# Performance work log

Hardware: AMD Instinct MI355X
Metric: run time of the kernel (lower is better)

The kernel has to match this reference:

```python
import jax, jax.numpy as jnp
import numpy as np

B, T, DIM, E, H = 128, 512, 256, 512, 512

def _linear_params(key, out_dim, in_dim, bias=True):
    k1, k2 = jax.random.split(key)
    bound = 1.0 / np.sqrt(in_dim)
    W = jax.random.uniform(k1, (out_dim, in_dim), jnp.float32, -bound, bound)
    if bias:
        b = jax.random.uniform(k2, (out_dim,), jnp.float32, -bound, bound)
        return W, b
    return W

def setup_inputs() -> dict:
    key = jax.random.key(0)
    ks = jax.random.split(key, 12)
    x_t = jax.random.normal(ks[0], (B, T, DIM), jnp.float32)
    h0 = jax.random.normal(ks[1], (B, H), jnp.float32)
    c0 = jax.random.normal(ks[2], (B, H), jnp.float32)
    We, be = _linear_params(ks[3], E, DIM)
    Wf, bf = _linear_params(ks[4], H, E)   # forget input proj
    Wi, bi = _linear_params(ks[5], H, E)   # input gate
    Wg, bg = _linear_params(ks[6], H, E)   # cell candidate
    Wo, bo = _linear_params(ks[7], H, E)   # output gate
    Rf = _linear_params(ks[8], H, H, bias=False)
    Ri = _linear_params(ks[9], H, H, bias=False)
    Rg = _linear_params(ks[10], H, H, bias=False)
    Ro = _linear_params(ks[11], H, H, bias=False)
    return dict(x_t=x_t, h0=h0, c0=c0, We=We, be=be,
                Wf=Wf, bf=bf, Wi=Wi, bi=bi, Wg=Wg, bg=bg, Wo=Wo, bo=bo,
                Rf=Rf, Ri=Ri, Rg=Rg, Ro=Ro)

def reference(x_t, h0, c0, We, be, Wf, bf, Wi, bi, Wg, bg, Wo, bo, Rf, Ri, Rg, Ro):
    # Embedding: [B,T,DIM] -> [B,T,E]
    xe = jnp.einsum('btd,ed->bte', x_t, We) + be
    # Batch all input-to-hidden projections across time in one GEMM each.
    xf = jnp.einsum('bte,he->bth', xe, Wf) + bf
    xi = jnp.einsum('bte,he->bth', xe, Wi) + bi
    xg = jnp.einsum('bte,he->bth', xe, Wg) + bg
    xo = jnp.einsum('bte,he->bth', xe, Wo) + bo
    xs = jnp.stack([xi, xf, xg, xo], axis=0)  # [4,B,T,H]

    def step(carry, x4):
        h, c = carry
        xi_t, xf_t, xg_t, xo_t = x4
        i = jax.nn.sigmoid(xi_t + h @ Ri.T)
        f = jax.nn.sigmoid(xf_t + h @ Rf.T)
        g = jnp.tanh(xg_t + h @ Rg.T)
        c_next = g * i + f * c
        o = jax.nn.sigmoid(xo_t + h @ Ro.T)
        h_next = o * jnp.tanh(c_next)
        return (h_next, c_next), h_next

    (h_last, c_last), hs = jax.lax.scan(step, (h0, c0), jnp.moveaxis(xs, 2, 0))
    hidden_seq = jnp.swapaxes(hs, 0, 1)  # [B,T,H]
    return hidden_seq, h_last, c_last
```

## Files before the change

### kernel.cpp

```cpp
#include <hip/hip_runtime.h>
#include <hip/hip_bf16.h>

#define B_ 128
#define T_ 512
#define DIM_ 256
#define E_ 512
#define H_ 512
#define NB_ 32
#define NG_ 8
#define WROW 1032

typedef __attribute__((ext_vector_type(8))) short short8;
typedef __attribute__((ext_vector_type(4))) float floatx4;
typedef unsigned long long ull_t;

__device__ __forceinline__ float sigmoidf_(float x) {
  return 1.0f / (1.0f + __expf(-x));
}

__device__ __forceinline__ short f2bs(float f) {
  __hip_bfloat16 h = __float2bfloat16(f);
  return *reinterpret_cast<short*>(&h);
}

__global__ __launch_bounds__(256) void cvt_we(const float* __restrict__ src,
                                              __hip_bfloat16* __restrict__ dst,
                                              int n) {
  int i = blockIdx.x * 256 + threadIdx.x;
  if (i < n) dst[i] = __float2bfloat16(src[i]);
}

__global__ __launch_bounds__(256) void embed_gemm(
    const float* __restrict__ A,
    const __hip_bfloat16* __restrict__ W,
    const float* __restrict__ bias,
    __hip_bfloat16* __restrict__ C)
{
  const int tid = threadIdx.x;
  const int lane = tid & 63;
  const int w = tid >> 6;
  const int q = lane >> 4;
  const int l15 = lane & 15;
  const int m0 = blockIdx.x * 32 + (w >> 1) * 16;
  const int n0 = (w & 1) * 256;

  const float* a_base = A + (size_t)(m0 + l15) * DIM_ + q * 8;

  floatx4 acc[16];
#pragma unroll
  for (int j = 0; j < 16; ++j) acc[j] = (floatx4){0.f, 0.f, 0.f, 0.f};

  for (int ks = 0; ks < 8; ++ks) {
    const float* ap = a_base + ks * 32;
    short8 a;
#pragma unroll
    for (int j = 0; j < 8; ++j) a[j] = f2bs(ap[j]);
    short8 bf[16];
#pragma unroll
    for (int j = 0; j < 16; ++j) {
      const short* b_ptr =
          (const short*)W + (n0 + j * 16 + l15) * DIM_ + ks * 32 + q * 8;
      bf[j] = *(const short8*)b_ptr;
    }
#pragma unroll
    for (int j = 0; j < 16; ++j)
      acc[j] = __builtin_amdgcn_mfma_f32_16x16x32_bf16(a, bf[j], acc[j], 0, 0, 0);
  }

#pragma unroll
  for (int j = 0; j < 16; ++j) {
    const int col = n0 + j * 16 + l15;
    const float bv = bias[col];
#pragma unroll
    for (int r = 0; r < 4; ++r) {
      const int row = m0 + q * 4 + r;
      C[(size_t)row * E_ + col] = __float2bfloat16(acc[j][r] + bv);
    }
  }
}

__device__ __forceinline__ void group_barrier(unsigned* cnt_g, unsigned target,
                                              int tid) {
  __syncthreads();
  if (tid == 0) {
    __hip_atomic_fetch_add(cnt_g, 1u, __ATOMIC_RELAXED,
                           __HIP_MEMORY_SCOPE_AGENT);
    while (__hip_atomic_load(cnt_g, __ATOMIC_RELAXED,
                             __HIP_MEMORY_SCOPE_AGENT) < target)
      __builtin_amdgcn_s_sleep(1);
  }
  __syncthreads();
}

__global__ __launch_bounds__(256, 1) void lstm_persist(
    const float* __restrict__ h0,
    const float* __restrict__ c0,
    const float* __restrict__ Wi_, const float* __restrict__ bi_,
    const float* __restrict__ Wf_, const float* __restrict__ bf_,
    const float* __restrict__ Wg_, const float* __restrict__ bg_,
    const float* __restrict__ Wo_, const float* __restrict__ bo_,
    const float* __restrict__ Ri_, const float* __restrict__ Rf_,
    const float* __restrict__ Rg_, const float* __restrict__ Ro_,
    const __hip_bfloat16* __restrict__ xe,
    unsigned* __restrict__ hbuf32,
    unsigned* __restrict__ cnt,
    float* __restrict__ out)
{
  extern __shared__ short wts[];
  __shared__ float pbuf[4][4][16][16];
  __shared__ float cbuf[16][16];
  __shared__ float bias_s[4][16];

  const int tid = threadIdx.x;
  const int lane = tid & 63;
  const int w = tid >> 6;
  const int q = lane >> 4;
  const int l15 = lane & 15;
  const int blk = blockIdx.x;
  const int g = blk & 7;
  const int jb = blk >> 3;
  const int b0 = g * 16;
  const int d0 = jb * 16;
  unsigned* cnt_g = cnt + g * 64;
  ull_t* hbuf64 = (ull_t*)hbuf32;

  const float* Wp[4] = {Wi_, Wf_, Wg_, Wo_};
  const float* Rp[4] = {Ri_, Rf_, Rg_, Ro_};
  const float* bp[4] = {bi_, bf_, bg_, bo_};

  for (int idx = tid; idx < 64 * 128; idx += 256) {
    const int row = idx >> 7;
    const int ch = idx & 127;
    const int G = row >> 4, dl = row & 15;
    const int k = ch * 8;
    const float* src = (k < 512) ? Wp[G] + (d0 + dl) * E_ + k
                                 : Rp[G] + (d0 + dl) * H_ + (k - 512);
    short8 v;
#pragma unroll
    for (int s = 0; s < 8; ++s) v[s] = f2bs(src[s]);
    *(short8*)&wts[row * WROW + k] = v;
  }
  if (tid < 64) {
    const int G = tid >> 4, n = tid & 15;
    bias_s[G][n] = bp[G][d0 + n];
  }
  {
    const int m = tid >> 4, n = tid & 15;
    cbuf[m][n] = c0[(b0 + m) * H_ + d0 + n];
  }
  if (tid < 128) {
    const int e = blk * 256 + tid * 2;
    unsigned pk = (unsigned)(unsigned short)f2bs(h0[e]) |
                  ((unsigned)(unsigned short)f2bs(h0[e + 1]) << 16);
    __hip_atomic_store(&hbuf32[blk * 128 + tid], pk, __ATOMIC_RELAXED,
                       __HIP_MEMORY_SCOPE_AGENT);
  }

  group_barrier(cnt_g, NB_, tid);

  const short* xbase = (const short*)xe +
      (size_t)(b0 + l15) * T_ * E_ + w * 256 + q * 8;

  const int lds_base = l15 * WROW + w * 256 + q * 8;

  short8 cur[8];
  if (w < 2) {
#pragma unroll
    for (int s = 0; s < 8; ++s) cur[s] = *(const short8*)(xbase + s * 32);
  }

  for (int t = 0; t < T_; ++t) {
    if (w >= 2) {
      const ull_t* hb = hbuf64 + (size_t)(t & 1) * (B_ * H_ / 4) +
                        (b0 + l15) * (H_ / 4) + (w - 2) * 64 + q * 2;
#pragma unroll
      for (int s = 0; s < 8; ++s) {
        union { ull_t u[2]; short8 v; } uu;
        uu.u[0] = __hip_atomic_load(hb + s * 8, __ATOMIC_RELAXED,
                                    __HIP_MEMORY_SCOPE_AGENT);
        uu.u[1] = __hip_atomic_load(hb + s * 8 + 1, __ATOMIC_RELAXED,
                                    __HIP_MEMORY_SCOPE_AGENT);
        cur[s] = uu.v;
      }
    }

    floatx4 acc[4];
#pragma unroll
    for (int G = 0; G < 4; ++G) acc[G] = (floatx4){0.f, 0.f, 0.f, 0.f};

#pragma unroll
    for (int s = 0; s < 8; ++s) {
#pragma unroll
      for (int G = 0; G < 4; ++G) {
        short8 b = *(const short8*)&wts[G * 16 * WROW + lds_base + s * 32];
        acc[G] = __builtin_amdgcn_mfma_f32_16x16x32_bf16(cur[s], b, acc[G], 0, 0, 0);
      }
    }

    if (w < 2 && t + 1 < T_) {
      const short* xp = xbase + (size_t)(t + 1) * E_;
#pragma unroll
      for (int s = 0; s < 8; ++s) cur[s] = *(const short8*)(xp + s * 32);
    }

#pragma unroll
    for (int G = 0; G < 4; ++G)
#pragma unroll
      for (int r = 0; r < 4; ++r)
        pbuf[w][G][q * 4 + r][l15] = acc[G][r];
    __syncthreads();

    {
      const int m = tid >> 4, n = tid & 15;
      float pre[4];
#pragma unroll
      for (int G = 0; G < 4; ++G)
        pre[G] = pbuf[0][G][m][n] + pbuf[1][G][m][n] + pbuf[2][G][m][n] +
                 pbuf[3][G][m][n] + bias_s[G][n];
      const float iv = sigmoidf_(pre[0]);
      const float fv = sigmoidf_(pre[1]);
      const float gv = tanhf(pre[2]);
      const float ov = sigmoidf_(pre[3]);
      const float c = gv * iv + fv * cbuf[m][n];
      cbuf[m][n] = c;
      const float h = ov * tanhf(c);

      unsigned hv = (unsigned)(unsigned short)f2bs(h);
      unsigned ov2 = __shfl_xor(hv, 1);
      if ((n & 1) == 0) {
        unsigned pk = hv | (ov2 << 16);
        __hip_atomic_store(
            &hbuf32[((t + 1) & 1) * (B_ * H_ / 2) + (b0 + m) * (H_ / 2) +
                    ((d0 + n) >> 1)],
            pk, __ATOMIC_RELAXED, __HIP_MEMORY_SCOPE_AGENT);
      }

      out[((size_t)(b0 + m) * T_ + t) * H_ + d0 + n] = h;
      if (t == T_ - 1) {
        out[(size_t)B_ * T_ * H_ + (b0 + m) * H_ + d0 + n] = h;
        out[(size_t)B_ * T_ * H_ + B_ * H_ + (b0 + m) * H_ + d0 + n] = c;
      }
    }

    group_barrier(cnt_g, NB_ * (t + 2), tid);
  }
}

extern "C" void kernel_launch(void* const* d_in, const int* in_sizes, int n_in,
                              void* d_out, int out_size, void* d_ws,
                              size_t ws_size, hipStream_t stream) {
  const float* x_t = (const float*)d_in[0];
  const float* h0  = (const float*)d_in[1];
  const float* c0  = (const float*)d_in[2];
  const float* We  = (const float*)d_in[3];
  const float* be  = (const float*)d_in[4];
  const float* Wf  = (const float*)d_in[5];
  const float* bf_ = (const float*)d_in[6];
  const float* Wi  = (const float*)d_in[7];
  const float* bi  = (const float*)d_in[8];
  const float* Wg  = (const float*)d_in[9];
  const float* bg  = (const float*)d_in[10];
  const float* Wo  = (const float*)d_in[11];
  const float* bo  = (const float*)d_in[12];
  const float* Rf  = (const float*)d_in[13];
  const float* Ri  = (const float*)d_in[14];
  const float* Rg  = (const float*)d_in[15];
  const float* Ro  = (const float*)d_in[16];
  float* out = (float*)d_out;

  char* ws = (char*)d_ws;
  unsigned* cnt = (unsigned*)ws;
  unsigned* hbuf = (unsigned*)(ws + 4096);
  __hip_bfloat16* Web  = (__hip_bfloat16*)(ws + 4096 + 262144);
  __hip_bfloat16* xe   = (__hip_bfloat16*)(ws + 4096 + 2 * 262144);

  hipMemsetAsync(cnt, 0, 2048, stream);

  cvt_we<<<(E_ * DIM_ + 255) / 256, 256, 0, stream>>>(We, Web, E_ * DIM_);

  embed_gemm<<<(B_ * T_) / 32, 256, 0, stream>>>(x_t, Web, be, xe);

  const size_t lds_bytes = 64 * WROW * sizeof(short);
  lstm_persist<<<NG_ * NB_, 256, lds_bytes, stream>>>(
      h0, c0, Wi, bi, Wf, bf_, Wg, bg, Wo, bo, Ri, Rf, Rg, Ro, xe, hbuf, cnt,
      out);
}
```

Baseline: 1.847 ms.

## Replace group counter barrier with per-block sequence flags and overlap input projection

Replaces the atomic-counter group barrier with per-block sequence flags that the recurrent waves poll directly, so only the waves that need h wait, and without sleep. The input-projection MFMAs for step t+1 are moved after the h publish, so they run while other blocks are still finishing step t. The output stores are deferred past the flag publish, and pbuf is padded to avoid LDS bank conflicts. Busy polling by 64 lanes raises memory traffic. Correctness depends on relaxed atomics giving enough ordering between the hbuf stores and the flag store.

```diff
diff --git a/kernel.cpp b/kernel.cpp
--- a/kernel.cpp
+++ b/kernel.cpp
@@ -79,19 +79,6 @@
   }
 }
 
-__device__ __forceinline__ void group_barrier(unsigned* cnt_g, unsigned target,
-                                              int tid) {
-  __syncthreads();
-  if (tid == 0) {
-    __hip_atomic_fetch_add(cnt_g, 1u, __ATOMIC_RELAXED,
-                           __HIP_MEMORY_SCOPE_AGENT);
-    while (__hip_atomic_load(cnt_g, __ATOMIC_RELAXED,
-                             __HIP_MEMORY_SCOPE_AGENT) < target)
-      __builtin_amdgcn_s_sleep(1);
-  }
-  __syncthreads();
-}
-
 __global__ __launch_bounds__(256, 1) void lstm_persist(
     const float* __restrict__ h0,
     const float* __restrict__ c0,
@@ -103,11 +90,11 @@
     const float* __restrict__ Rg_, const float* __restrict__ Ro_,
     const __hip_bfloat16* __restrict__ xe,
     unsigned* __restrict__ hbuf32,
-    unsigned* __restrict__ cnt,
+    unsigned* __restrict__ seq,
     float* __restrict__ out)
 {
   extern __shared__ short wts[];
-  __shared__ float pbuf[4][4][16][16];
+  __shared__ float pbuf[4][4][16][17];
   __shared__ float cbuf[16][16];
   __shared__ float bias_s[4][16];
 
@@ -121,7 +108,7 @@
   const int jb = blk >> 3;
   const int b0 = g * 16;
   const int d0 = jb * 16;
-  unsigned* cnt_g = cnt + g * 64;
+  unsigned* seq_g = seq + g * NB_;
   ull_t* hbuf64 = (ull_t*)hbuf32;
 
   const float* Wp[4] = {Wi_, Wf_, Wg_, Wo_};
@@ -149,14 +136,17 @@
     cbuf[m][n] = c0[(b0 + m) * H_ + d0 + n];
   }
   if (tid < 128) {
-    const int e = blk * 256 + tid * 2;
-    unsigned pk = (unsigned)(unsigned short)f2bs(h0[e]) |
-                  ((unsigned)(unsigned short)f2bs(h0[e + 1]) << 16);
-    __hip_atomic_store(&hbuf32[blk * 128 + tid], pk, __ATOMIC_RELAXED,
+    const int u = g * 4096 + jb * 128 + tid;
+    unsigned pk = (unsigned)(unsigned short)f2bs(h0[2 * u]) |
+                  ((unsigned)(unsigned short)f2bs(h0[2 * u + 1]) << 16);
+    __hip_atomic_store(&hbuf32[u], pk, __ATOMIC_RELAXED,
                        __HIP_MEMORY_SCOPE_AGENT);
   }
 
-  group_barrier(cnt_g, NB_, tid);
+  __syncthreads();
+  if (tid == 0)
+    __hip_atomic_store(&seq_g[jb], 1u, __ATOMIC_RELAXED,
+                       __HIP_MEMORY_SCOPE_AGENT);
 
   const short* xbase = (const short*)xe +
       (size_t)(b0 + l15) * T_ * E_ + w * 256 + q * 8;
@@ -167,65 +157,79 @@
   if (w < 2) {
 #pragma unroll
     for (int s = 0; s < 8; ++s) cur[s] = *(const short8*)(xbase + s * 32);
+    floatx4 acc[4];
+#pragma unroll
+    for (int G = 0; G < 4; ++G) acc[G] = (floatx4){0.f, 0.f, 0.f, 0.f};
+#pragma unroll
+    for (int s = 0; s < 8; ++s)
+#pragma unroll
+      for (int G = 0; G < 4; ++G) {
+        short8 bfr = *(const short8*)&wts[G * 16 * WROW + lds_base + s * 32];
+        acc[G] = __builtin_amdgcn_mfma_f32_16x16x32_bf16(cur[s], bfr, acc[G], 0, 0, 0);
+      }
+#pragma unroll
+    for (int G = 0; G < 4; ++G)
+#pragma unroll
+      for (int r = 0; r < 4; ++r)
+        pbuf[w][G][q * 4 + r][l15] = acc[G][r];
+#pragma unroll
+    for (int s = 0; s < 8; ++s) cur[s] = *(const short8*)(xbase + E_ + s * 32);
   }
 
   for (int t = 0; t < T_; ++t) {
     if (w >= 2) {
+      const unsigned tgt = (unsigned)(t + 1);
+      for (;;) {
+        unsigned v = __hip_atomic_load(&seq_g[lane & 31], __ATOMIC_RELAXED,
+                                       __HIP_MEMORY_SCOPE_AGENT);
+        if (__all((int)(v >= tgt))) break;
+      }
       const ull_t* hb = hbuf64 + (size_t)(t & 1) * (B_ * H_ / 4) +
                         (b0 + l15) * (H_ / 4) + (w - 2) * 64 + q * 2;
+      short8 hc[8];
 #pragma unroll
       for (int s = 0; s < 8; ++s) {
-        union { ull_t u[2]; short8 v; } uu;
+        union { ull_t u[2]; short8 v8; } uu;
         uu.u[0] = __hip_atomic_load(hb + s * 8, __ATOMIC_RELAXED,
                                     __HIP_MEMORY_SCOPE_AGENT);
         uu.u[1] = __hip_atomic_load(hb + s * 8 + 1, __ATOMIC_RELAXED,
                                     __HIP_MEMORY_SCOPE_AGENT);
-        cur[s] = uu.v;
-      }
-    }
-
-    floatx4 acc[4];
-#pragma unroll
-    for (int G = 0; G < 4; ++G) acc[G] = (floatx4){0.f, 0.f, 0.f, 0.f};
-
-#pragma unroll
-    for (int s = 0; s < 8; ++s) {
-#pragma unroll
-      for (int G = 0; G < 4; ++G) {
-        short8 b = *(const short8*)&wts[G * 16 * WROW + lds_base + s * 32];
-        acc[G] = __builtin_amdgcn_mfma_f32_16x16x32_bf16(cur[s], b, acc[G], 0, 0, 0);
-      }
-    }
-
-    if (w < 2 && t + 1 < T_) {
-      const short* xp = xbase + (size_t)(t + 1) * E_;
-#pragma unroll
-      for (int s = 0; s < 8; ++s) cur[s] = *(const short8*)(xp + s * 32);
-    }
-
+        hc[s] = uu.v8;
+      }
+      floatx4 acc[4];
+#pragma unroll
+      for (int G = 0; G < 4; ++G) acc[G] = (floatx4){0.f, 0.f, 0.f, 0.f};
+#pragma unroll
+      for (int s = 0; s < 8; ++s)
+#pragma unroll
+        for (int G = 0; G < 4; ++G) {
+          short8 bfr = *(const short8*)&wts[G * 16 * WROW + lds_base + s * 32];
+          acc[G] = __builtin_amdgcn_mfma_f32_16x16x32_bf16(hc[s], bfr, acc[G], 0, 0, 0);
+        }
+#pragma unroll
+      for (int G = 0; G < 4; ++G)
+#pragma unroll
+        for (int r = 0; r < 4; ++r)
+          pbuf[w][G][q * 4 + r][l15] = acc[G][r];
+    }
+    __syncthreads();
+
+    const int m = tid >> 4, n = tid & 15;
+    float pre[4];
 #pragma unroll
     for (int G = 0; G < 4; ++G)
-#pragma unroll
-      for (int r = 0; r < 4; ++r)
-        pbuf[w][G][q * 4 + r][l15] = acc[G][r];
-    __syncthreads();
+      pre[G] = pbuf[0][G][m][n] + pbuf[1][G][m][n] + pbuf[2][G][m][n] +
+               pbuf[3][G][m][n] + bias_s[G][n];
+    const float iv = sigmoidf_(pre[0]);
+    const float fv = sigmoidf_(pre[1]);
+    const float gv = tanhf(pre[2]);
+    const float ov = sigmoidf_(pre[3]);
+    const float c = gv * iv + fv * cbuf[m][n];
+    cbuf[m][n] = c;
+    const float hval = ov * tanhf(c);
 
     {
-      const int m = tid >> 4, n = tid & 15;
-      float pre[4];
-#pragma unroll
-      for (int G = 0; G < 4; ++G)
-        pre[G] = pbuf[0][G][m][n] + pbuf[1][G][m][n] + pbuf[2][G][m][n] +
-                 pbuf[3][G][m][n] + bias_s[G][n];
-      const float iv = sigmoidf_(pre[0]);
-      const float fv = sigmoidf_(pre[1]);
-      const float gv = tanhf(pre[2]);
-      const float ov = sigmoidf_(pre[3]);
-      const float c = gv * iv + fv * cbuf[m][n];
-      cbuf[m][n] = c;
-      const float h = ov * tanhf(c);
-
-      unsigned hv = (unsigned)(unsigned short)f2bs(h);
+      unsigned hv = (unsigned)(unsigned short)f2bs(hval);
       unsigned ov2 = __shfl_xor(hv, 1);
       if ((n & 1) == 0) {
         unsigned pk = hv | (ov2 << 16);
@@ -234,15 +238,40 @@
                     ((d0 + n) >> 1)],
             pk, __ATOMIC_RELAXED, __HIP_MEMORY_SCOPE_AGENT);
       }
-
-      out[((size_t)(b0 + m) * T_ + t) * H_ + d0 + n] = h;
-      if (t == T_ - 1) {
-        out[(size_t)B_ * T_ * H_ + (b0 + m) * H_ + d0 + n] = h;
-        out[(size_t)B_ * T_ * H_ + B_ * H_ + (b0 + m) * H_ + d0 + n] = c;
-      }
-    }
-
-    group_barrier(cnt_g, NB_ * (t + 2), tid);
+    }
+    __syncthreads();
+    if (tid == 0)
+      __hip_atomic_store(&seq_g[jb], (unsigned)(t + 2), __ATOMIC_RELAXED,
+                         __HIP_MEMORY_SCOPE_AGENT);
+
+    out[((size_t)(b0 + m) * T_ + t) * H_ + d0 + n] = hval;
+    if (t == T_ - 1) {
+      out[(size_t)B_ * T_ * H_ + (b0 + m) * H_ + d0 + n] = hval;
+      out[(size_t)B_ * T_ * H_ + B_ * H_ + (b0 + m) * H_ + d0 + n] = c;
+    }
+
+    if (w < 2 && t + 1 < T_) {
+      floatx4 acc[4];
+#pragma unroll
+      for (int G = 0; G < 4; ++G) acc[G] = (floatx4){0.f, 0.f, 0.f, 0.f};
+#pragma unroll
+      for (int s = 0; s < 8; ++s)
+#pragma unroll
+        for (int G = 0; G < 4; ++G) {
+          short8 bfr = *(const short8*)&wts[G * 16 * WROW + lds_base + s * 32];
+          acc[G] = __builtin_amdgcn_mfma_f32_16x16x32_bf16(cur[s], bfr, acc[G], 0, 0, 0);
+        }
+#pragma unroll
+      for (int G = 0; G < 4; ++G)
+#pragma unroll
+        for (int r = 0; r < 4; ++r)
+          pbuf[w][G][q * 4 + r][l15] = acc[G][r];
+      if (t + 2 < T_) {
+        const short* xp = xbase + (size_t)(t + 2) * E_;
+#pragma unroll
+        for (int s = 0; s < 8; ++s) cur[s] = *(const short8*)(xp + s * 32);
+      }
+    }
   }
 }
 
@@ -269,12 +298,12 @@
   float* out = (float*)d_out;
 
   char* ws = (char*)d_ws;
-  unsigned* cnt = (unsigned*)ws;
+  unsigned* seq  = (unsigned*)ws;
   unsigned* hbuf = (unsigned*)(ws + 4096);
   __hip_bfloat16* Web  = (__hip_bfloat16*)(ws + 4096 + 262144);
   __hip_bfloat16* xe   = (__hip_bfloat16*)(ws + 4096 + 2 * 262144);
 
-  hipMemsetAsync(cnt, 0, 2048, stream);
+  hipMemsetAsync(seq, 0, 4096, stream);
 
   cvt_we<<<(E_ * DIM_ + 255) / 256, 256, 0, stream>>>(We, Web, E_ * DIM_);
 
@@ -282,6 +311,6 @@
 
   const size_t lds_bytes = 64 * WROW * sizeof(short);
   lstm_persist<<<NG_ * NB_, 256, lds_bytes, stream>>>(
-      h0, c0, Wi, bi, Wf, bf_, Wg, bg, Wo, bo, Ri, Rf, Rg, Ro, xe, hbuf, cnt,
+      h0, c0, Wi, bi, Wf, bf_, Wg, bg, Wo, bo, Ri, Rf, Rg, Ro, xe, hbuf, seq,
       out);
 }
```

Result: slower. 2.281 ms (+23.5%).
